# Optimization experiments

Hardware: AMD Instinct MI355X
Metric: run time of the kernel (lower is better)

## Reference

```python
import jax, jax.numpy as jnp
import numpy as np

NUM_HEADS = 4
SPATIAL_DS = 2
EPS = 1e-5


def setup_inputs() -> dict:
    key = jax.random.key(0)
    ks = jax.random.split(key, 6)
    B, C, H, W = 8, 256, 64, 64
    hd = C // NUM_HEADS
    return {
        "x": jax.random.normal(ks[0], (B, C, H, W), jnp.float32),
        "gn_w": jnp.ones((C,), jnp.float32),
        "gn_b": jnp.zeros((C,), jnp.float32),
        "wq": jax.random.normal(ks[1], (C, C), jnp.float32) * (C ** -0.5),
        "wk": jax.random.normal(ks[2], (hd, C), jnp.float32) * (C ** -0.5),
        "wv": jax.random.normal(ks[3], (hd, C), jnp.float32) * (C ** -0.5),
        "wo": jax.random.normal(ks[4], (C, C), jnp.float32) * (C ** -0.5),
        "gamma": jnp.full((C,), 1e-4, jnp.float32),
    }


def reference(x, gn_w, gn_b, wq, wk, wv, wo, gamma):
    B, C, H, W = x.shape
    hd = C // NUM_HEADS
    scale = hd ** -0.5
    ds = SPATIAL_DS

    # GroupNorm with 1 group: normalize over (C,H,W) per sample, per-channel affine
    mu = jnp.mean(x, axis=(1, 2, 3), keepdims=True)
    var = jnp.var(x, axis=(1, 2, 3), keepdims=True)
    xn = (x - mu) * jax.lax.rsqrt(var + EPS)
    xn = xn * gn_w[None, :, None, None] + gn_b[None, :, None, None]

    # Q projection (1x1 conv == channel matmul): (B, heads, N, hd)
    q = jnp.einsum('oc,bchw->bohw', wq, xn).reshape(B, NUM_HEADS, hd, H * W)
    q = jnp.swapaxes(q, 2, 3)  # (B, h, N, hd)

    # AvgPool2d(ds, ds) on normalized input for K/V
    Hd, Wd = H // ds, W // ds
    x_ds = xn.reshape(B, C, Hd, ds, Wd, ds).mean(axis=(3, 5))

    k = jnp.einsum('oc,bchw->bohw', wk, x_ds).reshape(B, hd, Hd * Wd)
    k = jnp.swapaxes(k, 1, 2)  # (B, M, hd) single shared head
    v = jnp.einsum('oc,bchw->bohw', wv, x_ds).reshape(B, hd, Hd * Wd)
    v = jnp.swapaxes(v, 1, 2)  # (B, M, hd)

    # Multi-query attention: queries per-head, shared K/V
    attn = jnp.einsum('bhnd,bmd->bhnm', q, k) * scale
    attn = jax.nn.softmax(attn, axis=-1)
    out = jnp.einsum('bhnm,bmd->bhnd', attn, v)  # (B, h, N, hd)

    out = jnp.swapaxes(out, 2, 3).reshape(B, C, H, W)
    out = jnp.einsum('oc,bchw->bohw', wo, out)

    return x + out * gamma[None, :, None, None]
```

## Files before the change

kernel.cpp:

```cpp
#include <hip/hip_runtime.h>


#define CNT_INV (1.0f/1048576.0f)
#define EPSV 1e-5f
#define QSCALE 0.18033688f

#define WS_STATS 0
#define WS_XNT   64
#define WS_XDS   4194368
#define WS_K     5242944
#define WS_V     5505088
#define WS_WQB   5767232
#define WS_WKV   5800000
#define WS_WOB   5816384

typedef __attribute__((ext_vector_type(8))) short bf8_t;
typedef __attribute__((ext_vector_type(4))) float f4_t;

static __device__ __forceinline__ unsigned fbits(float f) {
  union { float f; unsigned u; } v; v.f = f; return v.u;
}
static __device__ __forceinline__ unsigned short f2bf(float f) {
  unsigned u = fbits(f);
  return (unsigned short)((u + 0x7fffu + ((u >> 16) & 1u)) >> 16);
}
static __device__ __forceinline__ unsigned pk_rnd(float a, float b) {
  return __builtin_amdgcn_perm(fbits(b) + 0x8000u, fbits(a) + 0x8000u, 0x07060302u);
}
static __device__ __forceinline__ unsigned pk_tr(float a, float b) {
  return __builtin_amdgcn_perm(fbits(b), fbits(a), 0x07060302u);
}
static __device__ __forceinline__ float bf2f(unsigned short h) {
  union { unsigned u; float f; } v; v.u = ((unsigned)h) << 16; return v.f;
}
static __device__ __forceinline__ float fexp2(float x) {
  float r; asm("v_exp_f32 %0, %1" : "=v"(r) : "v"(x)); return r;
}

__global__ __launch_bounds__(256) void k_prep_stats(const float* __restrict__ x,
                                                    const float* __restrict__ wq,
                                                    const float* __restrict__ wk,
                                                    const float* __restrict__ wv,
                                                    const float* __restrict__ wo,
                                                    float* __restrict__ stats,
                                                    unsigned short* __restrict__ wqb,
                                                    unsigned short* __restrict__ wkvb,
                                                    unsigned short* __restrict__ wob) {
  const int blk = blockIdx.x;
  const int t = threadIdx.x;
  if (blk < 512) {
    const int b = blk >> 6;
    const int chunk = blk & 63;
    const float4* xb = (const float4*)(x + (size_t)b * 1048576 + (size_t)chunk * 16384);
    float s = 0.f, s2 = 0.f;
#pragma unroll
    for (int it = 0; it < 16; ++it) {
      float4 v = xb[it * 256 + t];
      s  += v.x + v.y + v.z + v.w;
      s2 += v.x * v.x + v.y * v.y + v.z * v.z + v.w * v.w;
    }
#pragma unroll
    for (int o = 32; o > 0; o >>= 1) {
      s  += __shfl_down(s, o);
      s2 += __shfl_down(s2, o);
    }
    __shared__ float red[8];
    const int wid = t >> 6;
    if ((t & 63) == 0) { red[wid] = s; red[4 + wid] = s2; }
    __syncthreads();
    if (t == 0) {
      atomicAdd(&stats[b * 2 + 0], red[0] + red[1] + red[2] + red[3]);
      atomicAdd(&stats[b * 2 + 1], red[4] + red[5] + red[6] + red[7]);
    }
  } else {
    const int idx = (blk - 512) * 256 + t;
    if (idx < 65536) wqb[idx] = f2bf(wq[idx]);
    else if (idx < 81920) wkvb[idx - 65536] = f2bf(wk[idx - 65536]);
    else if (idx < 98304) wkvb[idx - 65536] = f2bf(wv[idx - 81920]);
    else if (idx < 163840) wob[idx - 98304] = f2bf(wo[idx - 98304]);
  }
}

__global__ __launch_bounds__(256) void k_xnt(const float* __restrict__ x,
                                             const float* __restrict__ gnw,
                                             const float* __restrict__ gnb,
                                             const float* __restrict__ stats,
                                             unsigned short* __restrict__ xnT,
                                             unsigned short* __restrict__ xdsT) {
  __shared__ unsigned short T[128][72];
  const int t = threadIdx.x;
  const int b = blockIdx.z, c0 = blockIdx.y * 64, hp = blockIdx.x;
  const int n0 = hp * 128;
  const float mu = stats[b * 2 + 0] * CNT_INV;
  const float rstd = rsqrtf(stats[b * 2 + 1] * CNT_INV - mu * mu + EPSV);
  const int n4 = (t & 31) * 4, cl = t >> 5;
#pragma unroll
  for (int p = 0; p < 8; ++p) {
    const int c = c0 + p * 8 + cl;
    const float gw = gnw[c] * rstd;
    const float gb = gnb[c] - mu * rstd * gnw[c];
    float4 v = *(const float4*)&x[(size_t)(b * 256 + c) * 4096 + n0 + n4];
    T[n4 + 0][p * 8 + cl] = f2bf(v.x * gw + gb);
    T[n4 + 1][p * 8 + cl] = f2bf(v.y * gw + gb);
    T[n4 + 2][p * 8 + cl] = f2bf(v.z * gw + gb);
    T[n4 + 3][p * 8 + cl] = f2bf(v.w * gw + gb);
  }
  __syncthreads();
  {
    const int r = t >> 1, ch = (t & 1) * 32;
    unsigned short* dst = xnT + ((size_t)b * 4096 + n0 + r) * 256 + c0 + ch;
#pragma unroll
    for (int u = 0; u < 4; ++u)
      *(uint4*)(dst + u * 8) = *(const uint4*)&T[r][ch + u * 8];
  }
  {
    const int wd = t & 31, c8 = (t >> 5) * 8;
    uint4 u0 = *(const uint4*)&T[2 * wd][c8];
    uint4 u1 = *(const uint4*)&T[2 * wd + 1][c8];
    uint4 u2 = *(const uint4*)&T[64 + 2 * wd][c8];
    uint4 u3 = *(const uint4*)&T[64 + 2 * wd + 1][c8];
    const unsigned* p0 = (const unsigned*)&u0; const unsigned* p1 = (const unsigned*)&u1;
    const unsigned* p2 = (const unsigned*)&u2; const unsigned* p3 = (const unsigned*)&u3;
    unsigned outp[4];
#pragma unroll
    for (int i = 0; i < 4; ++i) {
      float lo = (bf2f((unsigned short)p0[i]) + bf2f((unsigned short)p1[i]) +
                  bf2f((unsigned short)p2[i]) + bf2f((unsigned short)p3[i])) * 0.25f;
      float hi = (bf2f((unsigned short)(p0[i] >> 16)) + bf2f((unsigned short)(p1[i] >> 16)) +
                  bf2f((unsigned short)(p2[i] >> 16)) + bf2f((unsigned short)(p3[i] >> 16))) * 0.25f;
      outp[i] = pk_rnd(lo, hi);
    }
    *(uint4*)(xdsT + ((size_t)b * 1024 + hp * 32 + wd) * 256 + c0 + c8) = *(uint4*)outp;
  }
}

__global__ __launch_bounds__(256) void k_gemm_kv(const unsigned short* __restrict__ wkvb,
                                                 const unsigned short* __restrict__ xdsT,
                                                 unsigned short* __restrict__ kbf,
                                                 unsigned short* __restrict__ vtbf) {
  const int t = threadIdx.x;
  const int w = t >> 6, l = t & 63, lane16 = l & 15, quad = l >> 4;
  const int m0 = blockIdx.x * 64, b = blockIdx.y;
  const unsigned short* Abase = wkvb + (size_t)(w * 32 + lane16) * 256 + quad * 8;
  const unsigned short* Bbase = xdsT + ((size_t)b * 1024 + m0 + lane16) * 256 + quad * 8;
  f4_t acc[2][4];
#pragma unroll
  for (int i = 0; i < 2; ++i)
#pragma unroll
    for (int j = 0; j < 4; ++j) acc[i][j] = (f4_t){0.f, 0.f, 0.f, 0.f};
  bf8_t Ac[2], Bc[4];
#pragma unroll
  for (int og = 0; og < 2; ++og) Ac[og] = *(const bf8_t*)(Abase + (size_t)og * 16 * 256);
#pragma unroll
  for (int mg = 0; mg < 4; ++mg) Bc[mg] = *(const bf8_t*)(Bbase + (size_t)mg * 16 * 256);
  for (int kc = 0; kc < 256; kc += 32) {
    const int kn = (kc + 32) & 255;
    bf8_t An[2], Bn[4];
#pragma unroll
    for (int og = 0; og < 2; ++og) An[og] = *(const bf8_t*)(Abase + (size_t)og * 16 * 256 + kn);
#pragma unroll
    for (int mg = 0; mg < 4; ++mg) Bn[mg] = *(const bf8_t*)(Bbase + (size_t)mg * 16 * 256 + kn);
#pragma unroll
    for (int og = 0; og < 2; ++og)
#pragma unroll
      for (int mg = 0; mg < 4; ++mg)
        acc[og][mg] = __builtin_amdgcn_mfma_f32_16x16x32_bf16(Ac[og], Bc[mg], acc[og][mg], 0, 0, 0);
#pragma unroll
    for (int og = 0; og < 2; ++og) Ac[og] = An[og];
#pragma unroll
    for (int mg = 0; mg < 4; ++mg) Bc[mg] = Bn[mg];
  }
  if (w < 2) {
#pragma unroll
    for (int og = 0; og < 2; ++og)
#pragma unroll
      for (int mg = 0; mg < 4; ++mg) {
        const int m = m0 + mg * 16 + lane16;
        uint2 p;
        p.x = pk_rnd(acc[og][mg][0], acc[og][mg][1]);
        p.y = pk_rnd(acc[og][mg][2], acc[og][mg][3]);
        *(uint2*)(kbf + (size_t)b * 65536 + (size_t)m * 64 + w * 32 + og * 16 + quad * 4) = p;
      }
  } else {
#pragma unroll
    for (int og = 0; og < 2; ++og)
#pragma unroll
      for (int mg = 0; mg < 4; ++mg) {
        const int m = m0 + mg * 16 + lane16;
        const int d0 = (w - 2) * 32 + og * 16 + quad * 4;
#pragma unroll
        for (int r = 0; r < 4; ++r)
          vtbf[(size_t)b * 65536 + (size_t)(d0 + r) * 1024 + m] = f2bf(acc[og][mg][r]);
      }
  }
}

__global__ __launch_bounds__(256) void k_fused(const unsigned short* __restrict__ wqb,
                                               const unsigned short* __restrict__ xnT,
                                               const unsigned short* __restrict__ kbf,
                                               const unsigned short* __restrict__ vtbf,
                                               const unsigned short* __restrict__ wob,
                                               const float* __restrict__ x,
                                               const float* __restrict__ gamma,
                                               float* __restrict__ outp) {
  __shared__ __align__(16) unsigned short smem[20480];
  const int t = threadIdx.x;
  const int w = t >> 6, l = t & 63, lane16 = l & 15, quad = l >> 4;
  const int n0 = blockIdx.x * 64, b = blockIdx.y;
  const int h = w;
  unsigned short* qst = smem + w * 4608;
  unsigned short (*plds)[64][40] = (unsigned short (*)[64][40])(smem + w * 5120);
  unsigned short (*aos)[264] = (unsigned short (*)[264])smem;

  const unsigned short* kb = kbf + (size_t)b * 65536;
  const unsigned short* vb = vtbf + (size_t)b * 65536;

  {
    const unsigned short* Abase = wqb + (size_t)(h * 64 + lane16) * 256 + quad * 8;
    const unsigned short* Bbase = xnT + ((size_t)b * 4096 + n0 + lane16) * 256 + quad * 8;
    f4_t qacc[4][4];
#pragma unroll
    for (int i = 0; i < 4; ++i)
#pragma unroll
      for (int j = 0; j < 4; ++j) qacc[i][j] = (f4_t){0.f, 0.f, 0.f, 0.f};
    for (int kc = 0; kc < 256; kc += 32) {
      bf8_t A[4], Bf[4];
#pragma unroll
      for (int og = 0; og < 4; ++og) A[og] = *(const bf8_t*)(Abase + (size_t)og * 16 * 256 + kc);
#pragma unroll
      for (int ng = 0; ng < 4; ++ng) Bf[ng] = *(const bf8_t*)(Bbase + (size_t)ng * 16 * 256 + kc);
#pragma unroll
      for (int og = 0; og < 4; ++og)
#pragma unroll
        for (int ng = 0; ng < 4; ++ng)
          qacc[og][ng] = __builtin_amdgcn_mfma_f32_16x16x32_bf16(A[og], Bf[ng], qacc[og][ng], 0, 0, 0);
    }
#pragma unroll
    for (int og = 0; og < 4; ++og)
#pragma unroll
      for (int ng = 0; ng < 4; ++ng) {
        uint2 p;
        p.x = pk_rnd(qacc[og][ng][0] * QSCALE, qacc[og][ng][1] * QSCALE);
        p.y = pk_rnd(qacc[og][ng][2] * QSCALE, qacc[og][ng][3] * QSCALE);
        *(uint2*)&qst[(ng * 16 + lane16) * 72 + og * 16 + quad * 4] = p;
      }
  }
  bf8_t Qf[4][2];
#pragma unroll
  for (int qg = 0; qg < 4; ++qg)
#pragma unroll
    for (int dc = 0; dc < 2; ++dc)
      Qf[qg][dc] = *(const bf8_t*)&qst[(qg * 16 + lane16) * 72 + dc * 32 + quad * 8];
  __syncthreads();

  f4_t O[4][4];
#pragma unroll
  for (int dg = 0; dg < 4; ++dg)
#pragma unroll
    for (int qg = 0; qg < 4; ++qg) O[dg][qg] = (f4_t){0.f, 0.f, 0.f, 0.f};
  float den[4] = {0.f, 0.f, 0.f, 0.f};

#define SSTEP(KREG, BUF)                                                      \
  {                                                                           \
    _Pragma("unroll")                                                         \
    for (int qg = 0; qg < 4; ++qg) {                                          \
      _Pragma("unroll")                                                       \
      for (int s = 0; s < 2; ++s) {                                           \
        f4_t S = (f4_t){0.f, 0.f, 0.f, 0.f};                                  \
        S = __builtin_amdgcn_mfma_f32_16x16x32_bf16(KREG[s][0], Qf[qg][0], S, 0, 0, 0); \
        S = __builtin_amdgcn_mfma_f32_16x16x32_bf16(KREG[s][1], Qf[qg][1], S, 0, 0, 0); \
        float e0 = fexp2(S[0]);                                               \
        float e1 = fexp2(S[1]);                                               \
        float e2 = fexp2(S[2]);                                               \
        float e3 = fexp2(S[3]);                                               \
        den[qg] += (e0 + e1) + (e2 + e3);                                     \
        uint2 p; p.x = pk_tr(e0, e1); p.y = pk_tr(e2, e3);                    \
        *(uint2*)&plds[BUF][qg * 16 + lane16][s * 16 + quad * 4] = p;         \
      }                                                                       \
    }                                                                         \
  }

  bf8_t Kc[2][2];
#pragma unroll
  for (int s = 0; s < 2; ++s)
#pragma unroll
    for (int dc = 0; dc < 2; ++dc)
      Kc[s][dc] = *(const bf8_t*)(kb + (size_t)(s * 16 + lane16) * 64 + dc * 32 + quad * 8);
  SSTEP(Kc, 0);

  bf8_t Vc[4];
#pragma unroll
  for (int s = 0; s < 2; ++s)
#pragma unroll
    for (int dc = 0; dc < 2; ++dc)
      Kc[s][dc] = *(const bf8_t*)(kb + (size_t)(32 + s * 16 + lane16) * 64 + dc * 32 + quad * 8);
#pragma unroll
  for (int dg = 0; dg < 4; ++dg)
    Vc[dg] = *(const bf8_t*)(vb + (size_t)(dg * 16 + lane16) * 1024 + quad * 8);

  for (int it = 1; it < 32; ++it) {
    const int cb = it & 1, pb = cb ^ 1;
    bf8_t Pf[4];
#pragma unroll
    for (int qg = 0; qg < 4; ++qg)
      Pf[qg] = *(const bf8_t*)&plds[pb][qg * 16 + lane16][quad * 8];
    const int kvk = ((it + 1) & 31) * 32;
    const int kvv = it * 32;
    bf8_t K2[2][2], V2[4];
#pragma unroll
    for (int s = 0; s < 2; ++s)
#pragma unroll
      for (int dc = 0; dc < 2; ++dc)
        K2[s][dc] = *(const bf8_t*)(kb + (size_t)(kvk + s * 16 + lane16) * 64 + dc * 32 + quad * 8);
#pragma unroll
    for (int dg = 0; dg < 4; ++dg)
      V2[dg] = *(const bf8_t*)(vb + (size_t)(dg * 16 + lane16) * 1024 + kvv + quad * 8);
#pragma unroll
    for (int dg = 0; dg < 4; ++dg)
#pragma unroll
      for (int qg = 0; qg < 4; ++qg)
        O[dg][qg] = __builtin_amdgcn_mfma_f32_16x16x32_bf16(Vc[dg], Pf[qg], O[dg][qg], 0, 0, 0);
    SSTEP(Kc, cb);
#pragma unroll
    for (int s = 0; s < 2; ++s)
#pragma unroll
      for (int dc = 0; dc < 2; ++dc) Kc[s][dc] = K2[s][dc];
#pragma unroll
    for (int dg = 0; dg < 4; ++dg) Vc[dg] = V2[dg];
  }
  {
    bf8_t Pf[4];
#pragma unroll
    for (int qg = 0; qg < 4; ++qg)
      Pf[qg] = *(const bf8_t*)&plds[1][qg * 16 + lane16][quad * 8];
#pragma unroll
    for (int dg = 0; dg < 4; ++dg)
#pragma unroll
      for (int qg = 0; qg < 4; ++qg)
        O[dg][qg] = __builtin_amdgcn_mfma_f32_16x16x32_bf16(Vc[dg], Pf[qg], O[dg][qg], 0, 0, 0);
  }
#undef SSTEP

  float rden[4];
#pragma unroll
  for (int qg = 0; qg < 4; ++qg) {
    float d = den[qg];
    d += __shfl_xor(d, 16);
    d += __shfl_xor(d, 32);
    rden[qg] = 1.f / d;
  }

  __syncthreads();
#pragma unroll
  for (int dg = 0; dg < 4; ++dg)
#pragma unroll
    for (int qg = 0; qg < 4; ++qg) {
      const int c0 = h * 64 + dg * 16 + quad * 4;
      uint2 p;
      p.x = pk_rnd(O[dg][qg][0] * rden[qg], O[dg][qg][1] * rden[qg]);
      p.y = pk_rnd(O[dg][qg][2] * rden[qg], O[dg][qg][3] * rden[qg]);
      *(uint2*)&aos[qg * 16 + lane16][c0] = p;
    }
  __syncthreads();

  {
    const unsigned short* Wbase = wob + (size_t)(w * 64 + lane16) * 256 + quad * 8;
    f4_t acc[4][4];
#pragma unroll
    for (int i = 0; i < 4; ++i)
#pragma unroll
      for (int j = 0; j < 4; ++j) acc[i][j] = (f4_t){0.f, 0.f, 0.f, 0.f};
    for (int kc = 0; kc < 256; kc += 32) {
      bf8_t A[4], Bf[4];
#pragma unroll
      for (int og = 0; og < 4; ++og) A[og] = *(const bf8_t*)(Wbase + (size_t)og * 16 * 256 + kc);
#pragma unroll
      for (int ng = 0; ng < 4; ++ng) Bf[ng] = *(const bf8_t*)&aos[ng * 16 + lane16][kc + quad * 8];
#pragma unroll
      for (int og = 0; og < 4; ++og)
#pragma unroll
        for (int ng = 0; ng < 4; ++ng)
          acc[og][ng] = __builtin_amdgcn_mfma_f32_16x16x32_bf16(A[og], Bf[ng], acc[og][ng], 0, 0, 0);
    }
#pragma unroll
    for (int og = 0; og < 4; ++og) {
      float4 g4 = *(const float4*)&gamma[w * 64 + og * 16 + quad * 4];
      const float g[4] = {g4.x, g4.y, g4.z, g4.w};
#pragma unroll
      for (int ng = 0; ng < 4; ++ng) {
        const int n = n0 + ng * 16 + lane16;
#pragma unroll
        for (int r = 0; r < 4; ++r) {
          const int o = w * 64 + og * 16 + quad * 4 + r;
          const size_t ix = ((size_t)(b * 256 + o)) * 4096 + n;
          outp[ix] = x[ix] + g[r] * acc[og][ng][r];
        }
      }
    }
  }
}

extern "C" void kernel_launch(void* const* d_in, const int* in_sizes, int n_in,
                              void* d_out, int out_size, void* d_ws, size_t ws_size,
                              hipStream_t stream) {
  const float* x     = (const float*)d_in[0];
  const float* gnw   = (const float*)d_in[1];
  const float* gnb   = (const float*)d_in[2];
  const float* wq    = (const float*)d_in[3];
  const float* wk    = (const float*)d_in[4];
  const float* wv    = (const float*)d_in[5];
  const float* wo    = (const float*)d_in[6];
  const float* gamma = (const float*)d_in[7];
  float* out = (float*)d_out;
  float* ws  = (float*)d_ws;
  unsigned short* xnT  = (unsigned short*)(ws + WS_XNT);
  unsigned short* xdsT = (unsigned short*)(ws + WS_XDS);
  unsigned short* kbf  = (unsigned short*)(ws + WS_K);
  unsigned short* vtbf = (unsigned short*)(ws + WS_V);
  unsigned short* wqb  = (unsigned short*)(ws + WS_WQB);
  unsigned short* wkvb = (unsigned short*)(ws + WS_WKV);
  unsigned short* wob  = (unsigned short*)(ws + WS_WOB);

  hipMemsetAsync(ws, 0, 256, stream);
  k_prep_stats<<<1152, 256, 0, stream>>>(x, wq, wk, wv, wo, ws + WS_STATS, wqb, wkvb, wob);
  k_xnt<<<dim3(32, 4, 8), 256, 0, stream>>>(x, gnw, gnb, ws + WS_STATS, xnT, xdsT);
  k_gemm_kv<<<dim3(16, 8), 256, 0, stream>>>(wkvb, xdsT, kbf, vtbf);
  k_fused<<<dim3(64, 8), 256, 0, stream>>>(wqb, xnT, kbf, vtbf, wob, x, gamma, out);
}
```

Baseline: 217.0 us.

## Halve fused attention tile, compute softmax denominator via MFMA, stage K/V stores through LDS

The fused attention kernel now handles 32 queries per block instead of 64, giving twice as many blocks, smaller LDS, and a launch-bounds hint for four blocks per CU. The softmax denominator is now accumulated with an extra MFMA against a ones vector instead of scalar adds and shuffles. The main loop is reordered so the softmax step runs before the PV MFMAs, wrapped in setprio. The KV GEMM stages its outputs through shared memory for coalesced stores, and the downsample write index mapping in k_xnt changes. Smaller tiles re-stream K/V and weight data more often per query.

```diff
diff --git a/kernel.cpp b/kernel.cpp
--- a/kernel.cpp
+++ b/kernel.cpp
@@ -114,7 +114,7 @@
       *(uint4*)(dst + u * 8) = *(const uint4*)&T[r][ch + u * 8];
   }
   {
-    const int wd = t & 31, c8 = (t >> 5) * 8;
+    const int wd = t >> 3, c8 = (t & 7) * 8;
     uint4 u0 = *(const uint4*)&T[2 * wd][c8];
     uint4 u1 = *(const uint4*)&T[2 * wd + 1][c8];
     uint4 u2 = *(const uint4*)&T[64 + 2 * wd][c8];
@@ -138,6 +138,7 @@
                                                  const unsigned short* __restrict__ xdsT,
                                                  unsigned short* __restrict__ kbf,
                                                  unsigned short* __restrict__ vtbf) {
+  __shared__ __align__(16) unsigned short kv[2][64][72];
   const int t = threadIdx.x;
   const int w = t >> 6, l = t & 63, lane16 = l & 15, quad = l >> 4;
   const int m0 = blockIdx.x * 64, b = blockIdx.y;
@@ -175,41 +176,51 @@
     for (int og = 0; og < 2; ++og)
 #pragma unroll
       for (int mg = 0; mg < 4; ++mg) {
-        const int m = m0 + mg * 16 + lane16;
         uint2 p;
         p.x = pk_rnd(acc[og][mg][0], acc[og][mg][1]);
         p.y = pk_rnd(acc[og][mg][2], acc[og][mg][3]);
-        *(uint2*)(kbf + (size_t)b * 65536 + (size_t)m * 64 + w * 32 + og * 16 + quad * 4) = p;
+        *(uint2*)&kv[0][mg * 16 + lane16][w * 32 + og * 16 + quad * 4] = p;
       }
   } else {
 #pragma unroll
     for (int og = 0; og < 2; ++og)
 #pragma unroll
       for (int mg = 0; mg < 4; ++mg) {
-        const int m = m0 + mg * 16 + lane16;
         const int d0 = (w - 2) * 32 + og * 16 + quad * 4;
 #pragma unroll
         for (int r = 0; r < 4; ++r)
-          vtbf[(size_t)b * 65536 + (size_t)(d0 + r) * 1024 + m] = f2bf(acc[og][mg][r]);
+          kv[1][d0 + r][mg * 16 + lane16] = f2bf(acc[og][mg][r]);
       }
   }
-}
-
-__global__ __launch_bounds__(256) void k_fused(const unsigned short* __restrict__ wqb,
-                                               const unsigned short* __restrict__ xnT,
-                                               const unsigned short* __restrict__ kbf,
-                                               const unsigned short* __restrict__ vtbf,
-                                               const unsigned short* __restrict__ wob,
-                                               const float* __restrict__ x,
-                                               const float* __restrict__ gamma,
-                                               float* __restrict__ outp) {
-  __shared__ __align__(16) unsigned short smem[20480];
+  __syncthreads();
+  {
+    const int row = t >> 2, seg = (t & 3) * 16;
+    uint4 k0 = *(const uint4*)&kv[0][row][seg];
+    uint4 k1 = *(const uint4*)&kv[0][row][seg + 8];
+    unsigned short* kd = kbf + (size_t)b * 65536 + (size_t)(m0 + row) * 64 + seg;
+    *(uint4*)kd = k0; *(uint4*)(kd + 8) = k1;
+    uint4 v0 = *(const uint4*)&kv[1][row][seg];
+    uint4 v1 = *(const uint4*)&kv[1][row][seg + 8];
+    unsigned short* vd = vtbf + (size_t)b * 65536 + (size_t)row * 1024 + m0 + seg;
+    *(uint4*)vd = v0; *(uint4*)(vd + 8) = v1;
+  }
+}
+
+__global__ __launch_bounds__(256, 4) void k_fused(const unsigned short* __restrict__ wqb,
+                                                  const unsigned short* __restrict__ xnT,
+                                                  const unsigned short* __restrict__ kbf,
+                                                  const unsigned short* __restrict__ vtbf,
+                                                  const unsigned short* __restrict__ wob,
+                                                  const float* __restrict__ x,
+                                                  const float* __restrict__ gamma,
+                                                  float* __restrict__ outp) {
+  __shared__ __align__(16) unsigned short smem[10240];
   const int t = threadIdx.x;
   const int w = t >> 6, l = t & 63, lane16 = l & 15, quad = l >> 4;
-  const int n0 = blockIdx.x * 64, b = blockIdx.y;
+  const int n0 = blockIdx.x * 32, b = blockIdx.y;
   const int h = w;
-  unsigned short* qst = smem + w * 4608;
-  unsigned short (*plds)[64][40] = (unsigned short (*)[64][40])(smem + w * 5120);
+  unsigned short* qst = smem + w * 2304;
+  unsigned short (*plds)[32][40] = (unsigned short (*)[32][40])(smem + w * 2560);
   unsigned short (*aos)[264] = (unsigned short (*)[264])smem;
 
   const unsigned short* kb = kbf + (size_t)b * 65536;
@@ -218,52 +229,56 @@
   {
     const unsigned short* Abase = wqb + (size_t)(h * 64 + lane16) * 256 + quad * 8;
     const unsigned short* Bbase = xnT + ((size_t)b * 4096 + n0 + lane16) * 256 + quad * 8;
-    f4_t qacc[4][4];
+    f4_t qacc[4][2];
 #pragma unroll
     for (int i = 0; i < 4; ++i)
 #pragma unroll
-      for (int j = 0; j < 4; ++j) qacc[i][j] = (f4_t){0.f, 0.f, 0.f, 0.f};
+      for (int j = 0; j < 2; ++j) qacc[i][j] = (f4_t){0.f, 0.f, 0.f, 0.f};
     for (int kc = 0; kc < 256; kc += 32) {
-      bf8_t A[4], Bf[4];
+      bf8_t A[4], Bf[2];
 #pragma unroll
       for (int og = 0; og < 4; ++og) A[og] = *(const bf8_t*)(Abase + (size_t)og * 16 * 256 + kc);
 #pragma unroll
-      for (int ng = 0; ng < 4; ++ng) Bf[ng] = *(const bf8_t*)(Bbase + (size_t)ng * 16 * 256 + kc);
+      for (int ng = 0; ng < 2; ++ng) Bf[ng] = *(const bf8_t*)(Bbase + (size_t)ng * 16 * 256 + kc);
 #pragma unroll
       for (int og = 0; og < 4; ++og)
 #pragma unroll
-        for (int ng = 0; ng < 4; ++ng)
+        for (int ng = 0; ng < 2; ++ng)
           qacc[og][ng] = __builtin_amdgcn_mfma_f32_16x16x32_bf16(A[og], Bf[ng], qacc[og][ng], 0, 0, 0);
     }
 #pragma unroll
     for (int og = 0; og < 4; ++og)
 #pragma unroll
-      for (int ng = 0; ng < 4; ++ng) {
+      for (int ng = 0; ng < 2; ++ng) {
         uint2 p;
         p.x = pk_rnd(qacc[og][ng][0] * QSCALE, qacc[og][ng][1] * QSCALE);
         p.y = pk_rnd(qacc[og][ng][2] * QSCALE, qacc[og][ng][3] * QSCALE);
         *(uint2*)&qst[(ng * 16 + lane16) * 72 + og * 16 + quad * 4] = p;
       }
   }
-  bf8_t Qf[4][2];
-#pragma unroll
-  for (int qg = 0; qg < 4; ++qg)
+  bf8_t Qf[2][2];
+#pragma unroll
+  for (int qg = 0; qg < 2; ++qg)
 #pragma unroll
     for (int dc = 0; dc < 2; ++dc)
       Qf[qg][dc] = *(const bf8_t*)&qst[(qg * 16 + lane16) * 72 + dc * 32 + quad * 8];
   __syncthreads();
 
-  f4_t O[4][4];
+  f4_t O[4][2];
 #pragma unroll
   for (int dg = 0; dg < 4; ++dg)
 #pragma unroll
-    for (int qg = 0; qg < 4; ++qg) O[dg][qg] = (f4_t){0.f, 0.f, 0.f, 0.f};
-  float den[4] = {0.f, 0.f, 0.f, 0.f};
+    for (int qg = 0; qg < 2; ++qg) O[dg][qg] = (f4_t){0.f, 0.f, 0.f, 0.f};
+  f4_t O4[2];
+  O4[0] = (f4_t){0.f, 0.f, 0.f, 0.f};
+  O4[1] = (f4_t){0.f, 0.f, 0.f, 0.f};
+  const short onebf = (lane16 == 0) ? (short)0x3F80 : (short)0;
+  const bf8_t Aone = {onebf, onebf, onebf, onebf, onebf, onebf, onebf, onebf};
 
 #define SSTEP(KREG, BUF)                                                      \
   {                                                                           \
     _Pragma("unroll")                                                         \
-    for (int qg = 0; qg < 4; ++qg) {                                          \
+    for (int qg = 0; qg < 2; ++qg) {                                          \
       _Pragma("unroll")                                                       \
       for (int s = 0; s < 2; ++s) {                                           \
         f4_t S = (f4_t){0.f, 0.f, 0.f, 0.f};                                  \
@@ -273,22 +288,19 @@
         float e1 = fexp2(S[1]);                                               \
         float e2 = fexp2(S[2]);                                               \
         float e3 = fexp2(S[3]);                                               \
-        den[qg] += (e0 + e1) + (e2 + e3);                                     \
         uint2 p; p.x = pk_tr(e0, e1); p.y = pk_tr(e2, e3);                    \
         *(uint2*)&plds[BUF][qg * 16 + lane16][s * 16 + quad * 4] = p;         \
       }                                                                       \
     }                                                                         \
   }
 
-  bf8_t Kc[2][2];
+  bf8_t Kc[2][2], Vc[4];
 #pragma unroll
   for (int s = 0; s < 2; ++s)
 #pragma unroll
     for (int dc = 0; dc < 2; ++dc)
       Kc[s][dc] = *(const bf8_t*)(kb + (size_t)(s * 16 + lane16) * 64 + dc * 32 + quad * 8);
   SSTEP(Kc, 0);
-
-  bf8_t Vc[4];
 #pragma unroll
   for (int s = 0; s < 2; ++s)
 #pragma unroll
@@ -300,53 +312,54 @@
 
   for (int it = 1; it < 32; ++it) {
     const int cb = it & 1, pb = cb ^ 1;
-    bf8_t Pf[4];
-#pragma unroll
-    for (int qg = 0; qg < 4; ++qg)
+    bf8_t Pf[2];
+#pragma unroll
+    for (int qg = 0; qg < 2; ++qg)
       Pf[qg] = *(const bf8_t*)&plds[pb][qg * 16 + lane16][quad * 8];
+    SSTEP(Kc, cb);
     const int kvk = ((it + 1) & 31) * 32;
+#pragma unroll
+    for (int s = 0; s < 2; ++s)
+#pragma unroll
+      for (int dc = 0; dc < 2; ++dc)
+        Kc[s][dc] = *(const bf8_t*)(kb + (size_t)(kvk + s * 16 + lane16) * 64 + dc * 32 + quad * 8);
+    __builtin_amdgcn_s_setprio(1);
+#pragma unroll
+    for (int dg = 0; dg < 4; ++dg)
+#pragma unroll
+      for (int qg = 0; qg < 2; ++qg)
+        O[dg][qg] = __builtin_amdgcn_mfma_f32_16x16x32_bf16(Vc[dg], Pf[qg], O[dg][qg], 0, 0, 0);
+#pragma unroll
+    for (int qg = 0; qg < 2; ++qg)
+      O4[qg] = __builtin_amdgcn_mfma_f32_16x16x32_bf16(Aone, Pf[qg], O4[qg], 0, 0, 0);
+    __builtin_amdgcn_s_setprio(0);
     const int kvv = it * 32;
-    bf8_t K2[2][2], V2[4];
-#pragma unroll
-    for (int s = 0; s < 2; ++s)
-#pragma unroll
-      for (int dc = 0; dc < 2; ++dc)
-        K2[s][dc] = *(const bf8_t*)(kb + (size_t)(kvk + s * 16 + lane16) * 64 + dc * 32 + quad * 8);
 #pragma unroll
     for (int dg = 0; dg < 4; ++dg)
-      V2[dg] = *(const bf8_t*)(vb + (size_t)(dg * 16 + lane16) * 1024 + kvv + quad * 8);
+      Vc[dg] = *(const bf8_t*)(vb + (size_t)(dg * 16 + lane16) * 1024 + kvv + quad * 8);
+  }
+  {
+    bf8_t Pf[2];
+#pragma unroll
+    for (int qg = 0; qg < 2; ++qg)
+      Pf[qg] = *(const bf8_t*)&plds[1][qg * 16 + lane16][quad * 8];
+    __builtin_amdgcn_s_setprio(1);
 #pragma unroll
     for (int dg = 0; dg < 4; ++dg)
 #pragma unroll
-      for (int qg = 0; qg < 4; ++qg)
+      for (int qg = 0; qg < 2; ++qg)
         O[dg][qg] = __builtin_amdgcn_mfma_f32_16x16x32_bf16(Vc[dg], Pf[qg], O[dg][qg], 0, 0, 0);
-    SSTEP(Kc, cb);
-#pragma unroll
-    for (int s = 0; s < 2; ++s)
-#pragma unroll
-      for (int dc = 0; dc < 2; ++dc) Kc[s][dc] = K2[s][dc];
-#pragma unroll
-    for (int dg = 0; dg < 4; ++dg) Vc[dg] = V2[dg];
-  }
-  {
-    bf8_t Pf[4];
-#pragma unroll
-    for (int qg = 0; qg < 4; ++qg)
-      Pf[qg] = *(const bf8_t*)&plds[1][qg * 16 + lane16][quad * 8];
-#pragma unroll
-    for (int dg = 0; dg < 4; ++dg)
-#pragma unroll
-      for (int qg = 0; qg < 4; ++qg)
-        O[dg][qg] = __builtin_amdgcn_mfma_f32_16x16x32_bf16(Vc[dg], Pf[qg], O[dg][qg], 0, 0, 0);
+#pragma unroll
+    for (int qg = 0; qg < 2; ++qg)
+      O4[qg] = __builtin_amdgcn_mfma_f32_16x16x32_bf16(Aone, Pf[qg], O4[qg], 0, 0, 0);
+    __builtin_amdgcn_s_setprio(0);
   }
 #undef SSTEP
 
-  float rden[4];
-#pragma unroll
-  for (int qg = 0; qg < 4; ++qg) {
-    float d = den[qg];
-    d += __shfl_xor(d, 16);
-    d += __shfl_xor(d, 32);
+  float rden[2];
+#pragma unroll
+  for (int qg = 0; qg < 2; ++qg) {
+    float d = __shfl(O4[qg][0], lane16);
     rden[qg] = 1.f / d;
   }
 
@@ -354,7 +367,7 @@
 #pragma unroll
   for (int dg = 0; dg < 4; ++dg)
 #pragma unroll
-    for (int qg = 0; qg < 4; ++qg) {
+    for (int qg = 0; qg < 2; ++qg) {
       const int c0 = h * 64 + dg * 16 + quad * 4;
       uint2 p;
       p.x = pk_rnd(O[dg][qg][0] * rden[qg], O[dg][qg][1] * rden[qg]);
@@ -365,21 +378,21 @@
 
   {
     const unsigned short* Wbase = wob + (size_t)(w * 64 + lane16) * 256 + quad * 8;
-    f4_t acc[4][4];
+    f4_t acc[4][2];
 #pragma unroll
     for (int i = 0; i < 4; ++i)
 #pragma unroll
-      for (int j = 0; j < 4; ++j) acc[i][j] = (f4_t){0.f, 0.f, 0.f, 0.f};
+      for (int j = 0; j < 2; ++j) acc[i][j] = (f4_t){0.f, 0.f, 0.f, 0.f};
     for (int kc = 0; kc < 256; kc += 32) {
-      bf8_t A[4], Bf[4];
+      bf8_t A[4], Bf[2];
 #pragma unroll
       for (int og = 0; og < 4; ++og) A[og] = *(const bf8_t*)(Wbase + (size_t)og * 16 * 256 + kc);
 #pragma unroll
-      for (int ng = 0; ng < 4; ++ng) Bf[ng] = *(const bf8_t*)&aos[ng * 16 + lane16][kc + quad * 8];
+      for (int ng = 0; ng < 2; ++ng) Bf[ng] = *(const bf8_t*)&aos[ng * 16 + lane16][kc + quad * 8];
 #pragma unroll
       for (int og = 0; og < 4; ++og)
 #pragma unroll
-        for (int ng = 0; ng < 4; ++ng)
+        for (int ng = 0; ng < 2; ++ng)
           acc[og][ng] = __builtin_amdgcn_mfma_f32_16x16x32_bf16(A[og], Bf[ng], acc[og][ng], 0, 0, 0);
     }
 #pragma unroll
@@ -387,7 +400,7 @@
       float4 g4 = *(const float4*)&gamma[w * 64 + og * 16 + quad * 4];
       const float g[4] = {g4.x, g4.y, g4.z, g4.w};
 #pragma unroll
-      for (int ng = 0; ng < 4; ++ng) {
+      for (int ng = 0; ng < 2; ++ng) {
         const int n = n0 + ng * 16 + lane16;
 #pragma unroll
         for (int r = 0; r < 4; ++r) {
@@ -425,5 +438,5 @@
   k_prep_stats<<<1152, 256, 0, stream>>>(x, wq, wk, wv, wo, ws + WS_STATS, wqb, wkvb, wob);
   k_xnt<<<dim3(32, 4, 8), 256, 0, stream>>>(x, gnw, gnb, ws + WS_STATS, xnT, xdsT);
   k_gemm_kv<<<dim3(16, 8), 256, 0, stream>>>(wkvb, xdsT, kbf, vtbf);
-  k_fused<<<dim3(64, 8), 256, 0, stream>>>(wqb, xnT, kbf, vtbf, wob, x, gamma, out);
-}
+  k_fused<<<dim3(128, 8), 256, 0, stream>>>(wqb, xnT, kbf, vtbf, wob, x, gamma, out);
+}
```

Result: slower. 279.5 us (+28.8%).
